# Kernel optimization log

Hardware: AMD Instinct MI355X
Metric: run time of the kernel (lower is better)

## Reference

```python
import jax, jax.numpy as jnp
import numpy as np
import math

FS = 44100.0
HOP = 256
N_BANDS = 24
KS_BUF = 768  # > max delay 44100/60 = 735 samples


def _lpc1(x, a):
    # order-1 all-pole (sample_wise_lpc with order 1, per-batch constant coeff):
    # y[n] = x[n] - a*y[n-1];  x: [B,N], a: [B]
    def step(yp, xt):
        y = xt - a * yp
        return y, y
    _, ys = jax.lax.scan(step, jnp.zeros_like(a), x.T)
    return ys.T


def _diff_ks(f0_frames, exc, l_b):
    # differentiable Karplus-Strong: fractional-delay loop + 2-tap damping filter.
    # f0_frames: [B,F] Hz, exc: [B,N], l_b: [B,F,2] (loop_coeff, loop_mix logits)
    B, N = exc.shape
    g = 0.999 * jax.nn.sigmoid(l_b[..., 0])   # loop gain in (0, 0.999)
    s = jax.nn.sigmoid(l_b[..., 1])           # loop-filter mix
    up = lambda p: jnp.repeat(p, HOP, axis=1)[:, :N]
    g_s, s_s = up(g), up(s)
    f0_s = up(jnp.clip(f0_frames, 60.0, None))
    D = jnp.clip(FS / f0_s, 2.0, 735.0)        # delay in samples
    Di = jnp.floor(D).astype(jnp.int32)
    fr = (D - Di).astype(exc.dtype)
    L = KS_BUF

    def step(carry, xs):
        buf, n = carry                         # buf: [B,L] circular delay line
        x_t, Di_t, fr_t, g_t, s_t = xs         # each [B]
        i1 = jnp.mod(n - Di_t, L)
        i2 = jnp.mod(n - Di_t - 1, L)
        i3 = jnp.mod(n - Di_t - 2, L)
        take = lambda i: jnp.take_along_axis(buf, i[:, None], axis=1)[:, 0]
        b1, b2, b3 = take(i1), take(i2), take(i3)
        z = (1.0 - fr_t) * b1 + fr_t * b2      # fractional-delay read y[n-D]
        z1 = (1.0 - fr_t) * b2 + fr_t * b3     # y[n-D-1]
        y = x_t + g_t * ((1.0 - s_t) * z + s_t * z1)
        buf = buf.at[:, jnp.mod(n, L)].set(y)
        return (buf, n + 1), y

    xs = (exc.T, Di.T, fr.T, g_s.T, s_s.T)
    init = (jnp.zeros((B, L), exc.dtype), jnp.int32(0))
    _, ys = jax.lax.scan(step, init, xs)
    return ys.T


def _body(x, body_gains):
    # bank of 24 two-pole resonators, log-spaced 80..8000 Hz, Q=10
    fc = jnp.geomspace(80.0, 8000.0, N_BANDS).astype(x.dtype)
    w = 2.0 * jnp.pi * fc / FS
    r = jnp.exp(-jnp.pi * fc / (10.0 * FS))
    a1 = -2.0 * r * jnp.cos(w)
    a2 = r * r
    b0 = 1.0 - r
    B = x.shape[0]

    def step(carry, xt):
        y1, y2 = carry                          # [B,24] each
        y = b0 * xt[:, None] - a1 * y1 - a2 * y2
        return (y, y1), jnp.sum(y * body_gains, axis=-1)

    init = (jnp.zeros((B, N_BANDS), x.dtype), jnp.zeros((B, N_BANDS), x.dtype))
    _, out = jax.lax.scan(step, init, x.T)
    return out.T


def _forward(excitation, pitch, w1, b1, w2, b2, excitation_gain, body_gains):
    B, _, N = excitation.shape
    h = jax.nn.relu(pitch @ w1.T + b1)
    mlp_out = h @ w2.T + b2                     # [B,3]
    loop_coeff = jnp.clip(mlp_out[:, 0], -2.0, 2.5)
    loop_mix = jnp.clip(mlp_out[:, 1], -2.5, 0.0)
    frames = N // HOP
    l_b = jnp.broadcast_to(jnp.stack([loop_coeff, loop_mix], -1)[:, None, :], (B, frames, 2))
    f0_frames = jnp.broadcast_to(pitch, (B, frames))
    exc_sq = (excitation * excitation_gain)[:, 0, :]
    f0_hz = jnp.clip(pitch[:, 0], 60.0, None)
    mult = jnp.clip(2.0 + 6.0 * (f0_hz - 60.0) / 600.0, 2.0, 8.0)
    cutoff = jnp.minimum(2.0 * jnp.pi * f0_hz * mult / FS, jnp.pi * 0.9)
    alpha = 1.0 - jnp.exp(-cutoff)
    exc_f = _lpc1(exc_sq * alpha[:, None], alpha - 1.0)   # pre-KS one-pole LP
    string = _diff_ks(f0_frames, exc_f, l_b)
    loop_post = jnp.clip(mlp_out[:, 2], -4.0, 4.0)
    cutoff_post = jnp.minimum(jnp.pi * jax.nn.sigmoid(loop_post), jnp.pi * 0.99)
    alpha_p = 1.0 - jnp.exp(-cutoff_post)
    string = _lpc1(string * alpha_p[:, None], alpha_p - 1.0)  # post one-pole LP
    out = _body(string, body_gains)
    return out[:, None, :], loop_coeff.mean(), loop_mix.mean(), loop_post.mean()


def setup_inputs():
    key = jax.random.key(0)
    k = jax.random.split(key, 6)
    B, N = 8, 32768
    excitation = jax.random.normal(k[0], (B, 1, N), dtype=jnp.float32)
    pitch = 60.0 + 600.0 * jax.random.uniform(k[1], (B, 1), dtype=jnp.float32)
    bnd1 = 0.1 * math.sqrt(6.0 / (1 + 16))   # xavier_uniform, gain 0.1
    bnd2 = 0.1 * math.sqrt(6.0 / (16 + 3))
    w1 = jax.random.uniform(k[2], (16, 1), jnp.float32, -bnd1, bnd1)
    b1 = jnp.zeros((16,), jnp.float32)
    w2 = jax.random.uniform(k[3], (3, 16), jnp.float32, -bnd2, bnd2)
    b2 = jnp.array([0.9, 0.0, 0.0], jnp.float32)
    excitation_gain = jnp.array(0.25, jnp.float32)
    body_gains = 0.006 * jnp.ones((1, N_BANDS), jnp.float32)
    return {"excitation": excitation, "pitch": pitch, "w1": w1, "b1": b1,
            "w2": w2, "b2": b2, "excitation_gain": excitation_gain,
            "body_gains": body_gains}


def reference(excitation, pitch, w1, b1, w2, b2, excitation_gain, body_gains):
    return _forward(excitation, pitch, w1, b1, w2, b2, excitation_gain, body_gains)
```

## Files before the change

### kernel.cpp

```cpp
#include <hip/hip_runtime.h>
#include <math.h>

#define NSAMP 32768
#define FS_F 44100.0f
#define PI_F 3.14159265358979323846f
#define T1 1024
#define FLAG_MAGIC 0x5A5A5A5A

struct BParams {
  float alpha, alpha_p;
  float fr, g, s;
  int Di;
  float lc, lm, lp;
};

__device__ inline float sigmoidf_(float x) { return 1.0f / (1.0f + expf(-x)); }

__device__ inline BParams compute_params(int b, const float* __restrict__ pitch,
                                         const float* __restrict__ w1,
                                         const float* __restrict__ b1,
                                         const float* __restrict__ w2,
                                         const float* __restrict__ b2) {
  BParams P;
  float p = pitch[b];
  float h[16];
#pragma unroll
  for (int i = 0; i < 16; ++i) {
    float v = fmaf(p, w1[i], b1[i]);
    h[i] = v > 0.0f ? v : 0.0f;
  }
  float m[3];
#pragma unroll
  for (int j = 0; j < 3; ++j) {
    float acc = b2[j];
#pragma unroll
    for (int i = 0; i < 16; ++i) acc = fmaf(h[i], w2[j * 16 + i], acc);
    m[j] = acc;
  }
  P.lc = fminf(fmaxf(m[0], -2.0f), 2.5f);
  P.lm = fminf(fmaxf(m[1], -2.5f), 0.0f);
  P.lp = fminf(fmaxf(m[2], -4.0f), 4.0f);
  P.g = 0.999f * sigmoidf_(P.lc);
  P.s = sigmoidf_(P.lm);
  float f0 = fmaxf(p, 60.0f);
  float D = fminf(fmaxf(FS_F / f0, 2.0f), 735.0f);
  int Di = (int)floorf(D);
  P.fr = D - (float)Di;
  P.Di = Di;
  float mult = fminf(fmaxf(2.0f + 6.0f * (f0 - 60.0f) / 600.0f, 2.0f), 8.0f);
  float cutoff = fminf(2.0f * PI_F * f0 * mult / FS_F, PI_F * 0.9f);
  P.alpha = 1.0f - expf(-cutoff);
  float cpost = fminf(PI_F * sigmoidf_(P.lp), PI_F * 0.99f);
  P.alpha_p = 1.0f - expf(-cpost);
  return P;
}

__device__ inline float rl63(float v) {
  return __int_as_float(__builtin_amdgcn_readlane(__float_as_int(v), 63));
}
__device__ inline float rlv(float v, int l) {
  return __int_as_float(__builtin_amdgcn_readlane(__float_as_int(v), l));
}
__device__ inline float shr1(float v, float bnd) {
  return __int_as_float(__builtin_amdgcn_update_dpp(
      __float_as_int(bnd), __float_as_int(v), 0x138 , 0xf, 0xf,
      false));
}
__device__ inline float ror1(float v) {
  return __int_as_float(__builtin_amdgcn_update_dpp(
      __float_as_int(v), __float_as_int(v), 0x13C , 0xf, 0xf,
      false));
}

__device__ inline void barrier_lgkm() {
  asm volatile("s_waitcnt lgkmcnt(0)\n\ts_barrier" ::: "memory");
}

__device__ inline void band_coef(int k, float& a1, float& a2, float& b0) {
  float fc = 80.0f * exp2f((float)k * (6.64385618977472436f / 23.0f));
  float w = 2.0f * PI_F * fc / FS_F;
  float r = expf(-PI_F * fc / (10.0f * FS_F));
  a1 = -2.0f * r * cosf(w);
  a2 = r * r;
  b0 = 1.0f - r;
}

__device__ inline void gen_tables(float* __restrict__ tabs, int W) {
  if (W >= 120) return;
  const int j = W / 5, sub = W % 5;
  float A1, A2, B0;
  band_coef(j, A1, A2, B0);
  if (sub == 0) *(float4*)&tabs[j * 4] = make_float4(A1, A2, B0, 0.f);
  float Q00 = -A1, Q01 = -A2, Q10 = 1.f, Q11 = 0.f;
#pragma unroll
  for (int sq = 0; sq < 2; ++sq) {
    float n00 = fmaf(Q00, Q00, Q01 * Q10);
    float n01 = fmaf(Q00, Q01, Q01 * Q11);
    float n10 = fmaf(Q10, Q00, Q11 * Q10);
    float n11 = fmaf(Q10, Q01, Q11 * Q11);
    Q00 = n00; Q01 = n01; Q10 = n10; Q11 = n11;
  }
  float K00 = Q00, K01 = Q01, K10 = Q10, K11 = Q11;
#pragma unroll
  for (int sq = 0; sq < 2; ++sq) {
    float n00 = fmaf(Q00, Q00, Q01 * Q10);
    float n01 = fmaf(Q00, Q01, Q01 * Q11);
    float n10 = fmaf(Q10, Q00, Q11 * Q10);
    float n11 = fmaf(Q10, Q01, Q11 * Q11);
    Q00 = n00; Q01 = n01; Q10 = n10; Q11 = n11;
  }
  float L00[7], L01[7], L10[7], L11[7];
  L00[0] = fmaf(Q00, K00, Q01 * K10);
  L01[0] = fmaf(Q00, K01, Q01 * K11);
  L10[0] = fmaf(Q10, K00, Q11 * K10);
  L11[0] = fmaf(Q10, K01, Q11 * K11);
#pragma unroll
  for (int k = 0; k < 6; ++k) {
    float s00 = fmaf(L00[k], L00[k], L01[k] * L10[k]);
    float s01 = fmaf(L00[k], L01[k], L01[k] * L11[k]);
    float s10 = fmaf(L10[k], L00[k], L11[k] * L10[k]);
    float s11 = fmaf(L10[k], L01[k], L11[k] * L11[k]);
    L00[k + 1] = s00; L01[k + 1] = s01; L10[k + 1] = s10; L11[k + 1] = s11;
  }
  if (sub == 0) {
#pragma unroll
    for (int k = 0; k < 6; ++k)
      *(float4*)&tabs[96 + (k * 24 + j) * 4] =
          make_float4(L00[k], L01[k], L10[k], L11[k]);
    *(float4*)&tabs[672 + j * 4] = make_float4(L00[6], L01[6], L10[6], L11[6]);
  }
  int l0 = sub * 13, l1 = l0 + 13;
  if (l1 > 64) l1 = 64;
  for (int l = l0; l < l1; ++l) {
    float R00 = 1.f, R01 = 0.f, R10 = 0.f, R11 = 1.f;
#pragma unroll
    for (int bit = 0; bit < 6; ++bit) {
      if ((l >> bit) & 1) {
        float n00 = fmaf(L00[bit], R00, L01[bit] * R10);
        float n01 = fmaf(L00[bit], R01, L01[bit] * R11);
        float n10 = fmaf(L10[bit], R00, L11[bit] * R10);
        float n11 = fmaf(L10[bit], R01, L11[bit] * R11);
        R00 = n00; R01 = n01; R10 = n10; R11 = n11;
      }
    }
    *(float4*)&tabs[768 + (j * 64 + l) * 4] = make_float4(R00, R01, R10, R11);
  }
}

struct SCtx {
  const float* exc_b;
  float scale, c;
  float m1, m2, m4, m8, m16, m32, c512, c2048, c8lane, cgk;
  float vrun;
  int s1;
  float* lws;
};

__device__ inline void ld2(const float* __restrict__ p, int g0, float4& a,
                           float4& b) {
  a = make_float4(0.f, 0.f, 0.f, 0.f);
  b = make_float4(0.f, 0.f, 0.f, 0.f);
  if (g0 >= 0 && g0 + 3 < NSAMP) a = *(const float4*)&p[g0];
  if (g0 + 4 >= 0 && g0 + 7 < NSAMP) b = *(const float4*)&p[g0 + 4];
}

__device__ inline void scan_seg_pre(SCtx& SC, float* xbuf, int seg, bool write,
                                    int t, float4 xa, float4 xb) {
  const int lane = t & 63, wid = t >> 6;
  const int rel0 = seg << 11;
  barrier_lgkm();
  const float c = SC.c, scale = SC.scale;
  float S = 0.0f;
  S = fmaf(c, S, scale * xa.x); S = fmaf(c, S, scale * xa.y);
  S = fmaf(c, S, scale * xa.z); S = fmaf(c, S, scale * xa.w);
  S = fmaf(c, S, scale * xb.x); S = fmaf(c, S, scale * xb.y);
  S = fmaf(c, S, scale * xb.z); S = fmaf(c, S, scale * xb.w);
  float Sw = S, u;
  u = __shfl_up(Sw, 1);  if (lane >= 1)  Sw = fmaf(SC.m1, u, Sw);
  u = __shfl_up(Sw, 2);  if (lane >= 2)  Sw = fmaf(SC.m2, u, Sw);
  u = __shfl_up(Sw, 4);  if (lane >= 4)  Sw = fmaf(SC.m4, u, Sw);
  u = __shfl_up(Sw, 8);  if (lane >= 8)  Sw = fmaf(SC.m8, u, Sw);
  u = __shfl_up(Sw, 16); if (lane >= 16) Sw = fmaf(SC.m16, u, Sw);
  u = __shfl_up(Sw, 32); if (lane >= 32) Sw = fmaf(SC.m32, u, Sw);
  if (lane == 63) SC.lws[wid] = Sw;
  barrier_lgkm();
  float a0 = SC.lws[0], a1w = SC.lws[1], a2w = SC.lws[2], a3w = SC.lws[3];
  float carry = (wid == 1)   ? a0
                : (wid == 2) ? fmaf(SC.c512, a0, a1w)
                : (wid == 3) ? fmaf(SC.c512, fmaf(SC.c512, a0, a1w), a2w)
                             : 0.0f;
  float Sprev = __shfl_up(Sw, 1);
  float Sex = (lane == 0) ? 0.0f : Sprev;
  Sex = fmaf(SC.c8lane, carry, Sex);
  float v = fmaf(SC.cgk, SC.vrun, Sex);
  float4 ya, yb;
  v = fmaf(c, v, scale * xa.x); ya.x = v;
  v = fmaf(c, v, scale * xa.y); ya.y = v;
  v = fmaf(c, v, scale * xa.z); ya.z = v;
  v = fmaf(c, v, scale * xa.w); ya.w = v;
  v = fmaf(c, v, scale * xb.x); yb.x = v;
  v = fmaf(c, v, scale * xb.y); yb.y = v;
  v = fmaf(c, v, scale * xb.z); yb.z = v;
  v = fmaf(c, v, scale * xb.w); yb.w = v;
  if (write) {
    int o = (rel0 + 8 * t) & 8191;
    *(float4*)&xbuf[o] = ya;
    *(float4*)&xbuf[o + 4] = yb;
    if (o < 768) {
      *(float4*)&xbuf[o + 8192] = ya;
      *(float4*)&xbuf[o + 4 + 8192] = yb;
    }
  }
  float tS = fmaf(SC.c512, fmaf(SC.c512, fmaf(SC.c512, a0, a1w), a2w), a3w);
  SC.vrun = fmaf(SC.c2048, SC.vrun, tS);
}

__device__ inline void w1_load(const float* __restrict__ xg, int s1, int seg,
                               int lane, float4* pf) {
  const int base = s1 + (seg << 11) + (lane << 5);
#pragma unroll
  for (int i = 0; i < 8; ++i) {
    const int g = base + 4 * i;
    float4 v = make_float4(0.f, 0.f, 0.f, 0.f);
    if (g >= 0 && g + 3 < NSAMP) v = *(const float4*)&xg[g];
    pf[i] = v;
  }
}

template <int KNUM>
__device__ void ks_wave0(float* __restrict__ yg, const float* xbuf, int lane,
                         int C, float c0w, float c1w, float c2w, int s1,
                         int n0, int end, int span, int nseg) {
  const int lq1 = (C - 1) - (KNUM - 1) * 64;
  const int W = n0 - s1;
  float yp[KNUM], xC[KNUM], xN[KNUM];
  float p1 = 0.f, p2 = 0.f;
  int rel = 0;
#pragma unroll
  for (int k = 0; k < KNUM; ++k) { yp[k] = 0.f; xC[k] = 0.f; xN[k] = 0.f; }
  for (int s = 0; s < nseg; ++s) {
    barrier_lgkm();
    if (s == 0) {
#pragma unroll
      for (int k = 0; k < KNUM; ++k) {
        int i = lane + (k << 6);
        xC[k] = xbuf[i];
        xN[k] = xbuf[C + i];
      }
    }
    int fence = (s + 1) << 11;
    if (fence > span) fence = span;
    while (rel + C <= W && rel < fence) {
      float b2v[KNUM], b3v[KNUM];
      b2v[0] = shr1(yp[0], p1);
#pragma unroll
      for (int k = 1; k < KNUM; ++k) b2v[k] = shr1(yp[k], ror1(yp[k - 1]));
      b3v[0] = shr1(b2v[0], p2);
#pragma unroll
      for (int k = 1; k < KNUM; ++k) b3v[k] = shr1(b2v[k], ror1(b2v[k - 1]));
      float p1n = rlv(yp[KNUM - 1], lq1);
      float p2n = rlv(b2v[KNUM - 1], lq1);
#pragma unroll
      for (int k = 0; k < KNUM; ++k)
        yp[k] = fmaf(c0w, yp[k], fmaf(c2w, b3v[k], fmaf(c1w, b2v[k], xC[k])));
      p1 = p1n;
      p2 = p2n;
      const float* xp = &xbuf[((rel + 2 * C) & 8191) + lane];
#pragma unroll
      for (int k = 0; k < KNUM; ++k) {
        xC[k] = xN[k];
        xN[k] = xp[k << 6];
      }
      rel += C;
    }
    while (rel < fence) {
      float b2v[KNUM], b3v[KNUM];
      b2v[0] = shr1(yp[0], p1);
#pragma unroll
      for (int k = 1; k < KNUM; ++k) b2v[k] = shr1(yp[k], ror1(yp[k - 1]));
      b3v[0] = shr1(b2v[0], p2);
#pragma unroll
      for (int k = 1; k < KNUM; ++k) b3v[k] = shr1(b2v[k], ror1(b2v[k - 1]));
      float p1n = rlv(yp[KNUM - 1], lq1);
      float p2n = rlv(b2v[KNUM - 1], lq1);
#pragma unroll
      for (int k = 0; k < KNUM; ++k)
        yp[k] = fmaf(c0w, yp[k], fmaf(c2w, b3v[k], fmaf(c1w, b2v[k], xC[k])));
      p1 = p1n;
      p2 = p2n;
#pragma unroll
      for (int k = 0; k < KNUM; ++k) {
        int i = lane + (k << 6);
        int n = s1 + rel + i;
        bool okl = (k < KNUM - 1) || (lane <= lq1);
        if (okl && n >= n0 && n < end) yg[n] = yp[k];
      }
      const float* xp = &xbuf[((rel + 2 * C) & 8191) + lane];
#pragma unroll
      for (int k = 0; k < KNUM; ++k) {
        xC[k] = xN[k];
        xN[k] = xp[k << 6];
      }
      rel += C;
    }
  }
}

__device__ inline void ks_phase(int b, int q, const BParams& P,
                                const float* __restrict__ exc, float scale0,
                                float* __restrict__ buf1, float* xbuf,
                                float* lws, float* tabs, int t) {
  const int C = P.Di;
  const int n0 = q << 10;
  float lg = -logf(P.g);
  int Wp = (int)ceilf(10.5f / fmaxf(lg, 1e-6f));
  if (Wp > 64) Wp = 64;
  if (Wp < 4) Wp = 4;
  int W = Wp * C;
  if (W > n0) W = n0;
  W = (W + 3) & ~3;
  const int s1 = n0 - W;
  const int span = W + T1;
  const int end = n0 + T1;
  const int nseg = (span + 2047) >> 11;
  float* yg = buf1 + (size_t)b * NSAMP;

  SCtx SC;
  SC.exc_b = exc + (size_t)b * NSAMP;
  SC.c = 1.0f - P.alpha;
  SC.scale = scale0 * P.alpha;
  {
    float c = SC.c;
    float c2v = c * c, c4 = c2v * c2v, c8 = c4 * c4;
    SC.m1 = c8;
    SC.m2 = SC.m1 * SC.m1;
    SC.m4 = SC.m2 * SC.m2;
    SC.m8 = SC.m4 * SC.m4;
    SC.m16 = SC.m8 * SC.m8;
    SC.m32 = SC.m16 * SC.m16;
    SC.c512 = SC.m32 * SC.m32;
    float c1024 = SC.c512 * SC.c512;
    SC.c2048 = c1024 * c1024;
    float l2c = log2f(c);
    SC.c8lane = exp2f((float)(8 * (t & 63)) * l2c);
    SC.cgk = exp2f((float)(8 * t) * l2c);
  }
  SC.vrun = 0.0f;
  SC.s1 = s1;
  SC.lws = lws;

  const float* xg = SC.exc_b;
  float4 pA0, pB0, pA1, pB1, pA2, pB2, pA3, pB3;
  ld2(xg, s1 - 2048 + 8 * t, pA0, pB0);
  ld2(xg, s1 + 8 * t, pA1, pB1);
  ld2(xg, s1 + 2048 + 8 * t, pA2, pB2);
  ld2(xg, s1 + 4096 + 8 * t, pA3, pB3);
  scan_seg_pre(SC, xbuf, -1, false, t, pA0, pB0);
  scan_seg_pre(SC, xbuf, 0, true, t, pA1, pB1);
  scan_seg_pre(SC, xbuf, 1, true, t, pA2, pB2);
  scan_seg_pre(SC, xbuf, 2, true, t, pA3, pB3);

  const float c0w = P.g * (1.0f - P.s) * (1.0f - P.fr);
  const float c1w = P.g * ((1.0f - P.s) * P.fr + P.s * (1.0f - P.fr));
  const float c2w = P.g * P.s * P.fr;
  const int lane = t & 63, wid = t >> 6;

  if (wid == 0) {
    switch ((C + 63) >> 6) {
      case 2:  ks_wave0<2>(yg, xbuf, lane, C, c0w, c1w, c2w, s1, n0, end, span, nseg); break;
      case 3:  ks_wave0<3>(yg, xbuf, lane, C, c0w, c1w, c2w, s1, n0, end, span, nseg); break;
      case 4:  ks_wave0<4>(yg, xbuf, lane, C, c0w, c1w, c2w, s1, n0, end, span, nseg); break;
      case 5:  ks_wave0<5>(yg, xbuf, lane, C, c0w, c1w, c2w, s1, n0, end, span, nseg); break;
      case 6:  ks_wave0<6>(yg, xbuf, lane, C, c0w, c1w, c2w, s1, n0, end, span, nseg); break;
      case 7:  ks_wave0<7>(yg, xbuf, lane, C, c0w, c1w, c2w, s1, n0, end, span, nseg); break;
      case 8:  ks_wave0<8>(yg, xbuf, lane, C, c0w, c1w, c2w, s1, n0, end, span, nseg); break;
      case 9:  ks_wave0<9>(yg, xbuf, lane, C, c0w, c1w, c2w, s1, n0, end, span, nseg); break;
      case 10: ks_wave0<10>(yg, xbuf, lane, C, c0w, c1w, c2w, s1, n0, end, span, nseg); break;
      case 11: ks_wave0<11>(yg, xbuf, lane, C, c0w, c1w, c2w, s1, n0, end, span, nseg); break;
      default: ks_wave0<12>(yg, xbuf, lane, C, c0w, c1w, c2w, s1, n0, end, span, nseg); break;
    }
  } else if (wid == 1) {
    const float c = SC.c, scale = SC.scale;
    const float n1 = SC.m4, n2 = SC.m8, n4 = SC.m16, n8 = SC.m32;
    const float n16 = SC.c512, n32 = SC.c512 * SC.c512;
    const float c2048 = SC.c2048;
    const float c32lane = exp2f((float)(lane << 5) * log2f(c));
    float vrun = SC.vrun;
    float4 pf[8];
    w1_load(xg, s1, 3, lane, pf);
    for (int s = 0; s < nseg; ++s) {
      barrier_lgkm();
      const int ls = s + 3;
      if (ls < nseg) {
        float S = 0.0f;
#pragma unroll
        for (int i = 0; i < 8; ++i) {
          S = fmaf(c, S, scale * pf[i].x);
          S = fmaf(c, S, scale * pf[i].y);
          S = fmaf(c, S, scale * pf[i].z);
          S = fmaf(c, S, scale * pf[i].w);
        }
        float Sw = S, u;
        u = __shfl_up(Sw, 1);  if (lane >= 1)  Sw = fmaf(n1, u, Sw);
        u = __shfl_up(Sw, 2);  if (lane >= 2)  Sw = fmaf(n2, u, Sw);
        u = __shfl_up(Sw, 4);  if (lane >= 4)  Sw = fmaf(n4, u, Sw);
        u = __shfl_up(Sw, 8);  if (lane >= 8)  Sw = fmaf(n8, u, Sw);
        u = __shfl_up(Sw, 16); if (lane >= 16) Sw = fmaf(n16, u, Sw);
        u = __shfl_up(Sw, 32); if (lane >= 32) Sw = fmaf(n32, u, Sw);
        float tot = rlv(Sw, 63);
        float Sex = __shfl_up(Sw, 1);
        if (lane == 0) Sex = 0.0f;
        float v = fmaf(c32lane, vrun, Sex);
        const int o = ((ls << 11) & 8191) + (lane << 5);
#pragma unroll
        for (int i = 0; i < 8; ++i) {
          float4 y;
          v = fmaf(c, v, scale * pf[i].x); y.x = v;
          v = fmaf(c, v, scale * pf[i].y); y.y = v;
          v = fmaf(c, v, scale * pf[i].z); y.z = v;
          v = fmaf(c, v, scale * pf[i].w); y.w = v;
          *(float4*)&xbuf[o + 4 * i] = y;
          if (o + 4 * i < 768) *(float4*)&xbuf[o + 4 * i + 8192] = y;
        }
        vrun = fmaf(c2048, vrun, tot);
        w1_load(xg, s1, ls + 1, lane, pf);
      }
    }
  } else {
    barrier_lgkm();
    gen_tables(tabs, (wid - 2) * 64 + lane);
    for (int s = 1; s < nseg; ++s) barrier_lgkm();
  }
}

__device__ inline void lpc_lds(const float* __restrict__ xg,
                               float* __restrict__ sl, int s2, int nt, int lim,
                               float scale, float c, int t, float* lws) {
  const int lane = t & 63, wid = t >> 6;
  float c2v = c * c, c4 = c2v * c2v, c8 = c4 * c4;
  float m1 = c8, m2 = m1 * m1, m4 = m2 * m2, m8 = m4 * m4, m16 = m8 * m8,
        m32 = m16 * m16;
  float c512 = m32 * m32;
  float c2048 = c512 * c512;
  c2048 *= c2048;
  float l2c = log2f(c);
  float c8lane = exp2f((float)(8 * lane) * l2c);
  float cgk = exp2f((float)(8 * t) * l2c);
  float vrun = 0.0f;
  for (int tile = 0; tile < nt; ++tile) {
    __syncthreads();
    int g0 = s2 + (tile << 11) + 8 * t;
    float4 xa = make_float4(0.f, 0.f, 0.f, 0.f);
    float4 xb = make_float4(0.f, 0.f, 0.f, 0.f);
    if (g0 + 3 < lim) xa = *(const float4*)&xg[g0];
    if (g0 + 7 < lim) xb = *(const float4*)&xg[g0 + 4];
    float S = 0.0f;
    S = fmaf(c, S, scale * xa.x); S = fmaf(c, S, scale * xa.y);
    S = fmaf(c, S, scale * xa.z); S = fmaf(c, S, scale * xa.w);
    S = fmaf(c, S, scale * xb.x); S = fmaf(c, S, scale * xb.y);
    S = fmaf(c, S, scale * xb.z); S = fmaf(c, S, scale * xb.w);
    float Sw = S, u;
    u = __shfl_up(Sw, 1);  if (lane >= 1)  Sw = fmaf(m1, u, Sw);
    u = __shfl_up(Sw, 2);  if (lane >= 2)  Sw = fmaf(m2, u, Sw);
    u = __shfl_up(Sw, 4);  if (lane >= 4)  Sw = fmaf(m4, u, Sw);
    u = __shfl_up(Sw, 8);  if (lane >= 8)  Sw = fmaf(m8, u, Sw);
    u = __shfl_up(Sw, 16); if (lane >= 16) Sw = fmaf(m16, u, Sw);
    u = __shfl_up(Sw, 32); if (lane >= 32) Sw = fmaf(m32, u, Sw);
    if (lane == 63) lws[wid] = Sw;
    __syncthreads();
    float a0 = lws[0], a1w = lws[1], a2w = lws[2], a3w = lws[3];
    float carry = (wid == 1)   ? a0
                  : (wid == 2) ? fmaf(c512, a0, a1w)
                  : (wid == 3) ? fmaf(c512, fmaf(c512, a0, a1w), a2w)
                               : 0.0f;
    float Sprev = __shfl_up(Sw, 1);
    float Sex = (lane == 0) ? 0.0f : Sprev;
    Sex = fmaf(c8lane, carry, Sex);
    float v = fmaf(cgk, vrun, Sex);
    int o = g0 - s2;
    float4 ya, yb;
    v = fmaf(c, v, scale * xa.x); ya.x = v;
    v = fmaf(c, v, scale * xa.y); ya.y = v;
    v = fmaf(c, v, scale * xa.z); ya.z = v;
    v = fmaf(c, v, scale * xa.w); ya.w = v;
    v = fmaf(c, v, scale * xb.x); yb.x = v;
    v = fmaf(c, v, scale * xb.y); yb.y = v;
    v = fmaf(c, v, scale * xb.z); yb.z = v;
    v = fmaf(c, v, scale * xb.w); yb.w = v;
    *(float4*)&sl[o] = ya;
    *(float4*)&sl[o + 4] = yb;
    float tS = fmaf(c512, fmaf(c512, fmaf(c512, a0, a1w), a2w), a3w);
    vrun = fmaf(c2048, vrun, tS);
  }
}

__device__ inline void body_phase(int b, int q, const BParams& P,
                                  const float* __restrict__ gains,
                                  const float* __restrict__ buf1,
                                  float* __restrict__ out, float* sl,
                                  float* lws, float (*lc0)[8],
                                  float (*lc1)[8], const float* tabs, int t) {
  const int lane = t & 63, wid = t >> 6;
  const int n0 = q << 10;
  const int base = n0 - 4096;
  int s2 = base - 256;
  if (s2 < 0) s2 = 0;
  const int end = n0 + 1024;
  const int nt = (end - s2 + 2047) >> 11;

  lpc_lds(buf1 + (size_t)b * NSAMP, sl, s2, nt, end, P.alpha_p,
          1.0f - P.alpha_p, t, lws);
  __syncthreads();

  const float* bandcL = tabs;
  const float* QlevL = tabs + 96;
  const float* QwL = tabs + 672;
  const float* RtabL = tabs + 768;

  const int tb = base + 20 * t;
  float4 acc[5];
#pragma unroll
  for (int i = 0; i < 5; ++i) acc[i] = make_float4(0.f, 0.f, 0.f, 0.f);

  for (int g = 0; g < 3; ++g) {
    float A1[8], A2[8], B0[8], GN[8];
#pragma unroll
    for (int j = 0; j < 8; ++j) {
      int k = g * 8 + j;
      float4 bc = *(const float4*)&bandcL[k * 4];
      A1[j] = bc.x; A2[j] = bc.y; B0[j] = bc.z;
      GN[j] = gains[k];
    }
    float cv0[8], cv1[8];
#pragma unroll
    for (int j = 0; j < 8; ++j) cv0[j] = cv1[j] = 0.f;
    for (int i = 0; i < 5; ++i) {
      int n = tb + 4 * i;
      float4 xv = make_float4(0.f, 0.f, 0.f, 0.f);
      if (n >= 0) xv = *(const float4*)&sl[n - s2];
#pragma unroll
      for (int e = 0; e < 4; ++e) {
        float xi = e == 0 ? xv.x : e == 1 ? xv.y : e == 2 ? xv.z : xv.w;
#pragma unroll
        for (int j = 0; j < 8; ++j) {
          float nc = fmaf(B0[j], xi, -fmaf(A1[j], cv0[j], A2[j] * cv1[j]));
          cv1[j] = cv0[j];
          cv0[j] = nc;
        }
      }
    }
    int kl = 0;
    for (int off = 1; off <= 32; off <<= 1, ++kl) {
      float q00[8], q01[8], q10[8], q11[8];
#pragma unroll
      for (int j = 0; j < 8; ++j) {
        float4 qv = *(const float4*)&QlevL[(kl * 24 + g * 8 + j) * 4];
        q00[j] = qv.x; q01[j] = qv.y; q10[j] = qv.z; q11[j] = qv.w;
      }
#pragma unroll
      for (int j = 0; j < 8; ++j) {
        float u0 = __shfl_up(cv0[j], off);
        float u1 = __shfl_up(cv1[j], off);
        if (lane >= off) {
          float nc0 = fmaf(q00[j], u0, fmaf(q01[j], u1, cv0[j]));
          float nc1 = fmaf(q10[j], u0, fmaf(q11[j], u1, cv1[j]));
          cv0[j] = nc0;
          cv1[j] = nc1;
        }
      }
    }
    __syncthreads();
    if (lane == 63) {
#pragma unroll
      for (int j = 0; j < 8; ++j) {
        lc0[wid][j] = cv0[j];
        lc1[wid][j] = cv1[j];
      }
    }
    __syncthreads();
    float qw00[8], qw01[8], qw10[8], qw11[8];
#pragma unroll
    for (int j = 0; j < 8; ++j) {
      float4 qv = *(const float4*)&QwL[(g * 8 + j) * 4];
      qw00[j] = qv.x; qw01[j] = qv.y; qw10[j] = qv.z; qw11[j] = qv.w;
    }
    float car0[8], car1[8];
#pragma unroll
    for (int j = 0; j < 8; ++j) car0[j] = car1[j] = 0.f;
    for (int v = 0; v < wid; ++v) {
#pragma unroll
      for (int j = 0; j < 8; ++j) {
        float n0c = fmaf(qw00[j], car0[j], fmaf(qw01[j], car1[j], lc0[v][j]));
        float n1c = fmaf(qw10[j], car0[j], fmaf(qw11[j], car1[j], lc1[v][j]));
        car0[j] = n0c;
        car1[j] = n1c;
      }
    }
    float y1[8], y2[8];
#pragma unroll
    for (int j = 0; j < 8; ++j) {
      float4 rv = *(const float4*)&RtabL[((g * 8 + j) * 64 + lane) * 4];
      float e0 = __shfl_up(cv0[j], 1);
      float e1 = __shfl_up(cv1[j], 1);
      if (lane == 0) { e0 = 0.f; e1 = 0.f; }
      y1[j] = fmaf(rv.x, car0[j], fmaf(rv.y, car1[j], e0));
      y2[j] = fmaf(rv.z, car0[j], fmaf(rv.w, car1[j], e1));
    }
    if (tb + 20 > n0) {
      for (int i = 0; i < 5; ++i) {
        float4 xv = *(const float4*)&sl[tb - s2 + 4 * i];
        float4 ov = acc[i];
#pragma unroll
        for (int e = 0; e < 4; ++e) {
          float xi = e == 0 ? xv.x : e == 1 ? xv.y : e == 2 ? xv.z : xv.w;
          float a = 0.f;
#pragma unroll
          for (int j = 0; j < 8; ++j) {
            float yv = fmaf(B0[j], xi, -fmaf(A1[j], y1[j], A2[j] * y2[j]));
            y2[j] = y1[j];
            y1[j] = yv;
            a = fmaf(GN[j], yv, a);
          }
          if (e == 0) ov.x += a;
          else if (e == 1) ov.y += a;
          else if (e == 2) ov.z += a;
          else ov.w += a;
        }
        acc[i] = ov;
      }
    }
  }
  if (tb + 20 > n0) {
    float* outb = out + (size_t)b * NSAMP;
#pragma unroll
    for (int i = 0; i < 5; ++i) {
      int n = tb + 4 * i;
      if (n >= n0) *(float4*)&outb[n] = acc[i];
    }
  }
}

__global__ void __launch_bounds__(256, 1) synth_all(
    const float* __restrict__ exc, const float* __restrict__ pitch,
    const float* __restrict__ w1, const float* __restrict__ b1,
    const float* __restrict__ w2, const float* __restrict__ b2,
    const float* __restrict__ eg, const float* __restrict__ gains,
    float* __restrict__ buf1, int* __restrict__ flags,
    float* __restrict__ out) {
  const int blk = blockIdx.x;
  const int b = blk >> 5, q = blk & 31;
  const int t = threadIdx.x;
  __shared__ __align__(16) float smem[15888];

  BParams P = compute_params(b, pitch, w1, b1, w2, b2);
  if (blk == 0 && t < 64) {
    int bb = (t < 8) ? t : 0;
    BParams Q = compute_params(bb, pitch, w1, b1, w2, b2);
    float slc = 0.f, slm = 0.f, slp = 0.f;
    for (int i = 0; i < 8; ++i) {
      slc += rlv(Q.lc, i);
      slm += rlv(Q.lm, i);
      slp += rlv(Q.lp, i);
    }
    if (t == 0) {
      out[8 * NSAMP + 0] = slc / 8.0f;
      out[8 * NSAMP + 1] = slm / 8.0f;
      out[8 * NSAMP + 2] = slp / 8.0f;
    }
  }

  ks_phase(b, q, P, exc, eg[0], buf1, smem, smem + 8960, smem + 8976, t);
  __syncthreads();

  const int n0 = q << 10;
  int s2 = n0 - 4096 - 256;
  if (s2 < 0) s2 = 0;
  const int qlo = s2 >> 10;
  if (t == 0) {
    __hip_atomic_store(&flags[blk], FLAG_MAGIC, __ATOMIC_RELEASE,
                       __HIP_MEMORY_SCOPE_AGENT);
    for (int f = qlo; f < q; ++f) {
      while (__hip_atomic_load(&flags[b * 32 + f], __ATOMIC_ACQUIRE,
                               __HIP_MEMORY_SCOPE_AGENT) != FLAG_MAGIC) {
        __builtin_amdgcn_s_sleep(8);
      }
    }
  }
  __syncthreads();

  body_phase(b, q, P, gains, buf1, out, smem, smem + 6144,
             (float(*)[8])(smem + 6152), (float(*)[8])(smem + 6184),
             smem + 8976, t);
}

extern "C" void kernel_launch(void* const* d_in, const int* in_sizes, int n_in,
                              void* d_out, int out_size, void* d_ws, size_t ws_size,
                              hipStream_t stream) {
  const float* exc = (const float*)d_in[0];
  const float* pitch = (const float*)d_in[1];
  const float* w1 = (const float*)d_in[2];
  const float* b1 = (const float*)d_in[3];
  const float* w2 = (const float*)d_in[4];
  const float* b2 = (const float*)d_in[5];
  const float* eg = (const float*)d_in[6];
  const float* bg = (const float*)d_in[7];
  float* out = (float*)d_out;
  float* buf1 = (float*)d_ws;
  int* flags = (int*)(buf1 + 8 * NSAMP);

  hipLaunchKernelGGL(synth_all, dim3(256), dim3(256), 0, stream, exc, pitch,
                     w1, b1, w2, b2, eg, bg, buf1, flags, out);
}
```

Baseline: 114.4 us.

## Precompute full LPC-filtered excitation into large LDS before Karplus-Strong loop

Replaces the per-segment producer/consumer pipeline, in which wave 1 scanned the LPC filter into an 8K ring buffer while wave 0 ran the KS recurrence with per-segment barriers, with a two-pass parallel scan. All four waves first compute the whole filtered excitation span into a ~131KB dynamic LDS buffer, then apply inter-segment carry corrections. Only after that does wave 0 run the KS loop, with no barriers and no ring-buffer wrap. This removes barrier stalls and ring indexing from the serial loop. In exchange the LPC work is no longer overlapped with the KS recurrence, and the kernel now needs much more LDS.

```diff
diff --git a/kernel.cpp b/kernel.cpp
--- a/kernel.cpp
+++ b/kernel.cpp
@@ -6,6 +6,11 @@
 #define PI_F 3.14159265358979323846f
 #define T1 1024
 #define FLAG_MAGIC 0x5A5A5A5A
+
+#define XCAP 33536
+#define LWS_OFF 33536
+#define TABS_OFF 33568
+#define SMEM_FLOATS 40480
 
 struct BParams {
   float alpha, alpha_p;
@@ -55,9 +60,6 @@
   return P;
 }
 
-__device__ inline float rl63(float v) {
-  return __int_as_float(__builtin_amdgcn_readlane(__float_as_int(v), 63));
-}
 __device__ inline float rlv(float v, int l) {
   return __int_as_float(__builtin_amdgcn_readlane(__float_as_int(v), l));
 }
@@ -70,10 +72,6 @@
   return __int_as_float(__builtin_amdgcn_update_dpp(
       __float_as_int(v), __float_as_int(v), 0x13C , 0xf, 0xf,
       false));
-}
-
-__device__ inline void barrier_lgkm() {
-  asm volatile("s_waitcnt lgkmcnt(0)\n\ts_barrier" ::: "memory");
 }
 
 __device__ inline void band_coef(int k, float& a1, float& a2, float& b0) {
@@ -147,168 +145,91 @@
   }
 }
 
-struct SCtx {
-  const float* exc_b;
-  float scale, c;
-  float m1, m2, m4, m8, m16, m32, c512, c2048, c8lane, cgk;
-  float vrun;
-  int s1;
-  float* lws;
-};
-
-__device__ inline void ld2(const float* __restrict__ p, int g0, float4& a,
-                           float4& b) {
-  a = make_float4(0.f, 0.f, 0.f, 0.f);
-  b = make_float4(0.f, 0.f, 0.f, 0.f);
-  if (g0 >= 0 && g0 + 3 < NSAMP) a = *(const float4*)&p[g0];
-  if (g0 + 4 >= 0 && g0 + 7 < NSAMP) b = *(const float4*)&p[g0 + 4];
-}
-
-__device__ inline void scan_seg_pre(SCtx& SC, float* xbuf, int seg, bool write,
-                                    int t, float4 xa, float4 xb) {
-  const int lane = t & 63, wid = t >> 6;
-  const int rel0 = seg << 11;
-  barrier_lgkm();
-  const float c = SC.c, scale = SC.scale;
-  float S = 0.0f;
-  S = fmaf(c, S, scale * xa.x); S = fmaf(c, S, scale * xa.y);
-  S = fmaf(c, S, scale * xa.z); S = fmaf(c, S, scale * xa.w);
-  S = fmaf(c, S, scale * xb.x); S = fmaf(c, S, scale * xb.y);
-  S = fmaf(c, S, scale * xb.z); S = fmaf(c, S, scale * xb.w);
-  float Sw = S, u;
-  u = __shfl_up(Sw, 1);  if (lane >= 1)  Sw = fmaf(SC.m1, u, Sw);
-  u = __shfl_up(Sw, 2);  if (lane >= 2)  Sw = fmaf(SC.m2, u, Sw);
-  u = __shfl_up(Sw, 4);  if (lane >= 4)  Sw = fmaf(SC.m4, u, Sw);
-  u = __shfl_up(Sw, 8);  if (lane >= 8)  Sw = fmaf(SC.m8, u, Sw);
-  u = __shfl_up(Sw, 16); if (lane >= 16) Sw = fmaf(SC.m16, u, Sw);
-  u = __shfl_up(Sw, 32); if (lane >= 32) Sw = fmaf(SC.m32, u, Sw);
-  if (lane == 63) SC.lws[wid] = Sw;
-  barrier_lgkm();
-  float a0 = SC.lws[0], a1w = SC.lws[1], a2w = SC.lws[2], a3w = SC.lws[3];
-  float carry = (wid == 1)   ? a0
-                : (wid == 2) ? fmaf(SC.c512, a0, a1w)
-                : (wid == 3) ? fmaf(SC.c512, fmaf(SC.c512, a0, a1w), a2w)
-                             : 0.0f;
-  float Sprev = __shfl_up(Sw, 1);
-  float Sex = (lane == 0) ? 0.0f : Sprev;
-  Sex = fmaf(SC.c8lane, carry, Sex);
-  float v = fmaf(SC.cgk, SC.vrun, Sex);
-  float4 ya, yb;
-  v = fmaf(c, v, scale * xa.x); ya.x = v;
-  v = fmaf(c, v, scale * xa.y); ya.y = v;
-  v = fmaf(c, v, scale * xa.z); ya.z = v;
-  v = fmaf(c, v, scale * xa.w); ya.w = v;
-  v = fmaf(c, v, scale * xb.x); yb.x = v;
-  v = fmaf(c, v, scale * xb.y); yb.y = v;
-  v = fmaf(c, v, scale * xb.z); yb.z = v;
-  v = fmaf(c, v, scale * xb.w); yb.w = v;
-  if (write) {
-    int o = (rel0 + 8 * t) & 8191;
-    *(float4*)&xbuf[o] = ya;
-    *(float4*)&xbuf[o + 4] = yb;
-    if (o < 768) {
-      *(float4*)&xbuf[o + 8192] = ya;
-      *(float4*)&xbuf[o + 4 + 8192] = yb;
-    }
-  }
-  float tS = fmaf(SC.c512, fmaf(SC.c512, fmaf(SC.c512, a0, a1w), a2w), a3w);
-  SC.vrun = fmaf(SC.c2048, SC.vrun, tS);
-}
-
-__device__ inline void w1_load(const float* __restrict__ xg, int s1, int seg,
-                               int lane, float4* pf) {
-  const int base = s1 + (seg << 11) + (lane << 5);
-#pragma unroll
-  for (int i = 0; i < 8; ++i) {
-    const int g = base + 4 * i;
-    float4 v = make_float4(0.f, 0.f, 0.f, 0.f);
-    if (g >= 0 && g + 3 < NSAMP) v = *(const float4*)&xg[g];
-    pf[i] = v;
-  }
-}
-
 template <int KNUM>
-__device__ void ks_wave0(float* __restrict__ yg, const float* xbuf, int lane,
+__device__ void ks_wave0(float* __restrict__ yg, const float* xall, int lane,
                          int C, float c0w, float c1w, float c2w, int s1,
-                         int n0, int end, int span, int nseg) {
+                         int n0, int end, int span) {
   const int lq1 = (C - 1) - (KNUM - 1) * 64;
   const int W = n0 - s1;
   float yp[KNUM], xC[KNUM], xN[KNUM];
   float p1 = 0.f, p2 = 0.f;
+#pragma unroll
+  for (int k = 0; k < KNUM; ++k) {
+    yp[k] = 0.f;
+    xC[k] = xall[lane + (k << 6)];
+    xN[k] = xall[C + lane + (k << 6)];
+  }
   int rel = 0;
-#pragma unroll
-  for (int k = 0; k < KNUM; ++k) { yp[k] = 0.f; xC[k] = 0.f; xN[k] = 0.f; }
-  for (int s = 0; s < nseg; ++s) {
-    barrier_lgkm();
-    if (s == 0) {
-#pragma unroll
-      for (int k = 0; k < KNUM; ++k) {
-        int i = lane + (k << 6);
-        xC[k] = xbuf[i];
-        xN[k] = xbuf[C + i];
-      }
-    }
-    int fence = (s + 1) << 11;
-    if (fence > span) fence = span;
-    while (rel + C <= W && rel < fence) {
-      float b2v[KNUM], b3v[KNUM];
-      b2v[0] = shr1(yp[0], p1);
-#pragma unroll
-      for (int k = 1; k < KNUM; ++k) b2v[k] = shr1(yp[k], ror1(yp[k - 1]));
-      b3v[0] = shr1(b2v[0], p2);
-#pragma unroll
-      for (int k = 1; k < KNUM; ++k) b3v[k] = shr1(b2v[k], ror1(b2v[k - 1]));
-      float p1n = rlv(yp[KNUM - 1], lq1);
-      float p2n = rlv(b2v[KNUM - 1], lq1);
-#pragma unroll
-      for (int k = 0; k < KNUM; ++k)
-        yp[k] = fmaf(c0w, yp[k], fmaf(c2w, b3v[k], fmaf(c1w, b2v[k], xC[k])));
-      p1 = p1n;
-      p2 = p2n;
-      const float* xp = &xbuf[((rel + 2 * C) & 8191) + lane];
+  while (rel + C <= W) {
+    float b2v[KNUM], b3v[KNUM];
+    b2v[0] = shr1(yp[0], p1);
+#pragma unroll
+    for (int k = 1; k < KNUM; ++k) b2v[k] = shr1(yp[k], ror1(yp[k - 1]));
+    b3v[0] = shr1(b2v[0], p2);
+#pragma unroll
+    for (int k = 1; k < KNUM; ++k) b3v[k] = shr1(b2v[k], ror1(b2v[k - 1]));
+    float p1n = rlv(yp[KNUM - 1], lq1);
+    float p2n = rlv(b2v[KNUM - 1], lq1);
+#pragma unroll
+    for (int k = 0; k < KNUM; ++k)
+      yp[k] = fmaf(c0w, yp[k], fmaf(c2w, b3v[k], fmaf(c1w, b2v[k], xC[k])));
+    p1 = p1n;
+    p2 = p2n;
+    int r2 = rel + 2 * C;
+    if (r2 < span) {
+      const float* xp = &xall[r2 + lane];
 #pragma unroll
       for (int k = 0; k < KNUM; ++k) {
         xC[k] = xN[k];
         xN[k] = xp[k << 6];
       }
-      rel += C;
-    }
-    while (rel < fence) {
-      float b2v[KNUM], b3v[KNUM];
-      b2v[0] = shr1(yp[0], p1);
-#pragma unroll
-      for (int k = 1; k < KNUM; ++k) b2v[k] = shr1(yp[k], ror1(yp[k - 1]));
-      b3v[0] = shr1(b2v[0], p2);
-#pragma unroll
-      for (int k = 1; k < KNUM; ++k) b3v[k] = shr1(b2v[k], ror1(b2v[k - 1]));
-      float p1n = rlv(yp[KNUM - 1], lq1);
-      float p2n = rlv(b2v[KNUM - 1], lq1);
-#pragma unroll
-      for (int k = 0; k < KNUM; ++k)
-        yp[k] = fmaf(c0w, yp[k], fmaf(c2w, b3v[k], fmaf(c1w, b2v[k], xC[k])));
-      p1 = p1n;
-      p2 = p2n;
-#pragma unroll
-      for (int k = 0; k < KNUM; ++k) {
-        int i = lane + (k << 6);
-        int n = s1 + rel + i;
-        bool okl = (k < KNUM - 1) || (lane <= lq1);
-        if (okl && n >= n0 && n < end) yg[n] = yp[k];
-      }
-      const float* xp = &xbuf[((rel + 2 * C) & 8191) + lane];
+    } else {
+#pragma unroll
+      for (int k = 0; k < KNUM; ++k) xC[k] = xN[k];
+    }
+    rel += C;
+  }
+  while (rel < span) {
+    float b2v[KNUM], b3v[KNUM];
+    b2v[0] = shr1(yp[0], p1);
+#pragma unroll
+    for (int k = 1; k < KNUM; ++k) b2v[k] = shr1(yp[k], ror1(yp[k - 1]));
+    b3v[0] = shr1(b2v[0], p2);
+#pragma unroll
+    for (int k = 1; k < KNUM; ++k) b3v[k] = shr1(b2v[k], ror1(b2v[k - 1]));
+    float p1n = rlv(yp[KNUM - 1], lq1);
+    float p2n = rlv(b2v[KNUM - 1], lq1);
+#pragma unroll
+    for (int k = 0; k < KNUM; ++k)
+      yp[k] = fmaf(c0w, yp[k], fmaf(c2w, b3v[k], fmaf(c1w, b2v[k], xC[k])));
+    p1 = p1n;
+    p2 = p2n;
+#pragma unroll
+    for (int k = 0; k < KNUM; ++k) {
+      int i = lane + (k << 6);
+      int n = s1 + rel + i;
+      bool okl = (k < KNUM - 1) || (lane <= lq1);
+      if (okl && n >= n0 && n < end) yg[n] = yp[k];
+    }
+    int r2 = rel + 2 * C;
+    if (r2 < span) {
+      const float* xp = &xall[r2 + lane];
 #pragma unroll
       for (int k = 0; k < KNUM; ++k) {
         xC[k] = xN[k];
         xN[k] = xp[k << 6];
       }
-      rel += C;
-    }
+    } else {
+#pragma unroll
+      for (int k = 0; k < KNUM; ++k) xC[k] = xN[k];
+    }
+    rel += C;
   }
 }
 
 __device__ inline void ks_phase(int b, int q, const BParams& P,
                                 const float* __restrict__ exc, float scale0,
-                                float* __restrict__ buf1, float* xbuf,
+                                float* __restrict__ buf1, float* xall,
                                 float* lws, float* tabs, int t) {
   const int C = P.Di;
   const int n0 = q << 10;
@@ -322,114 +243,122 @@
   const int s1 = n0 - W;
   const int span = W + T1;
   const int end = n0 + T1;
-  const int nseg = (span + 2047) >> 11;
+  const int NSG = (span + 2047) >> 11;
   float* yg = buf1 + (size_t)b * NSAMP;
-
-  SCtx SC;
-  SC.exc_b = exc + (size_t)b * NSAMP;
-  SC.c = 1.0f - P.alpha;
-  SC.scale = scale0 * P.alpha;
+  const float* xg = exc + (size_t)b * NSAMP;
+
+  const float c = 1.0f - P.alpha;
+  const float scale = scale0 * P.alpha;
+  const float c2v = c * c, c4 = c2v * c2v, c8 = c4 * c4, c16 = c8 * c8;
+  const float c32 = c16 * c16, c64 = c32 * c32, c128 = c64 * c64;
+  const float c256 = c128 * c128, c512 = c256 * c256, c1024 = c512 * c512;
+  const float c2048 = c1024 * c1024;
+  const int lane = t & 63, wid = t >> 6;
+  const float c32lane = exp2f((float)(lane << 5) * log2f(c));
+
+  for (int r = 0; r < 5; ++r) {
+    int si = r * 4 + wid;
+    if (si > NSG) break;
+    int sg = si - 1;
+    int gbase = s1 + (sg << 11) + (lane << 5);
+    float4 pf[8];
+#pragma unroll
+    for (int i = 0; i < 8; ++i) {
+      int g = gbase + 4 * i;
+      float4 v = make_float4(0.f, 0.f, 0.f, 0.f);
+      if (g >= 0 && g + 3 < NSAMP) v = *(const float4*)&xg[g];
+      pf[i] = v;
+    }
+    float S = 0.0f;
+#pragma unroll
+    for (int i = 0; i < 8; ++i) {
+      S = fmaf(c, S, scale * pf[i].x);
+      S = fmaf(c, S, scale * pf[i].y);
+      S = fmaf(c, S, scale * pf[i].z);
+      S = fmaf(c, S, scale * pf[i].w);
+    }
+    float Sw = S, u;
+    u = __shfl_up(Sw, 1);  if (lane >= 1)  Sw = fmaf(c32, u, Sw);
+    u = __shfl_up(Sw, 2);  if (lane >= 2)  Sw = fmaf(c64, u, Sw);
+    u = __shfl_up(Sw, 4);  if (lane >= 4)  Sw = fmaf(c128, u, Sw);
+    u = __shfl_up(Sw, 8);  if (lane >= 8)  Sw = fmaf(c256, u, Sw);
+    u = __shfl_up(Sw, 16); if (lane >= 16) Sw = fmaf(c512, u, Sw);
+    u = __shfl_up(Sw, 32); if (lane >= 32) Sw = fmaf(c1024, u, Sw);
+    float tot = rlv(Sw, 63);
+    float Sex = __shfl_up(Sw, 1);
+    if (lane == 0) Sex = 0.0f;
+    if (lane == 0) lws[si] = tot;
+    if (sg >= 0) {
+      float v = Sex;
+#pragma unroll
+      for (int i = 0; i < 8; ++i) {
+        float4 y;
+        v = fmaf(c, v, scale * pf[i].x); y.x = v;
+        v = fmaf(c, v, scale * pf[i].y); y.y = v;
+        v = fmaf(c, v, scale * pf[i].z); y.z = v;
+        v = fmaf(c, v, scale * pf[i].w); y.w = v;
+        pf[i] = y;
+      }
+      int o = (sg << 11) + (lane << 5);
+#pragma unroll
+      for (int i = 0; i < 8; ++i) {
+        int ci = (lane + i) & 7;
+        *(float4*)&xall[o + 4 * ci] = pf[ci];
+      }
+    }
+  }
+  if (4 * t < 768) {
+    *(float4*)&xall[(NSG << 11) + 4 * t] = make_float4(0.f, 0.f, 0.f, 0.f);
+  }
+  __syncthreads();
   {
-    float c = SC.c;
-    float c2v = c * c, c4 = c2v * c2v, c8 = c4 * c4;
-    SC.m1 = c8;
-    SC.m2 = SC.m1 * SC.m1;
-    SC.m4 = SC.m2 * SC.m2;
-    SC.m8 = SC.m4 * SC.m4;
-    SC.m16 = SC.m8 * SC.m8;
-    SC.m32 = SC.m16 * SC.m16;
-    SC.c512 = SC.m32 * SC.m32;
-    float c1024 = SC.c512 * SC.c512;
-    SC.c2048 = c1024 * c1024;
-    float l2c = log2f(c);
-    SC.c8lane = exp2f((float)(8 * (t & 63)) * l2c);
-    SC.cgk = exp2f((float)(8 * t) * l2c);
-  }
-  SC.vrun = 0.0f;
-  SC.s1 = s1;
-  SC.lws = lws;
-
-  const float* xg = SC.exc_b;
-  float4 pA0, pB0, pA1, pB1, pA2, pB2, pA3, pB3;
-  ld2(xg, s1 - 2048 + 8 * t, pA0, pB0);
-  ld2(xg, s1 + 8 * t, pA1, pB1);
-  ld2(xg, s1 + 2048 + 8 * t, pA2, pB2);
-  ld2(xg, s1 + 4096 + 8 * t, pA3, pB3);
-  scan_seg_pre(SC, xbuf, -1, false, t, pA0, pB0);
-  scan_seg_pre(SC, xbuf, 0, true, t, pA1, pB1);
-  scan_seg_pre(SC, xbuf, 1, true, t, pA2, pB2);
-  scan_seg_pre(SC, xbuf, 2, true, t, pA3, pB3);
+    float p4[8];
+    p4[0] = 1.0f;
+#pragma unroll
+    for (int i = 1; i < 8; ++i) p4[i] = p4[i - 1] * c4;
+    for (int r = 0; r < 5; ++r) {
+      int si = r * 4 + wid;
+      if (si > NSG) break;
+      int sg = si - 1;
+      if (sg < 0) continue;
+      float vr = 0.0f;
+      for (int i = 0; i < si; ++i) vr = fmaf(c2048, vr, lws[i]);
+      float corr0 = c * (c32lane * vr);
+      int o = (sg << 11) + (lane << 5);
+#pragma unroll
+      for (int i = 0; i < 8; ++i) {
+        int ci = (lane + i) & 7;
+        float4 y = *(float4*)&xall[o + 4 * ci];
+        float f = corr0 * p4[ci];
+        y.x += f; f *= c;
+        y.y += f; f *= c;
+        y.z += f; f *= c;
+        y.w += f;
+        *(float4*)&xall[o + 4 * ci] = y;
+      }
+    }
+  }
+  __syncthreads();
 
   const float c0w = P.g * (1.0f - P.s) * (1.0f - P.fr);
   const float c1w = P.g * ((1.0f - P.s) * P.fr + P.s * (1.0f - P.fr));
   const float c2w = P.g * P.s * P.fr;
-  const int lane = t & 63, wid = t >> 6;
-
   if (wid == 0) {
     switch ((C + 63) >> 6) {
-      case 2:  ks_wave0<2>(yg, xbuf, lane, C, c0w, c1w, c2w, s1, n0, end, span, nseg); break;
-      case 3:  ks_wave0<3>(yg, xbuf, lane, C, c0w, c1w, c2w, s1, n0, end, span, nseg); break;
-      case 4:  ks_wave0<4>(yg, xbuf, lane, C, c0w, c1w, c2w, s1, n0, end, span, nseg); break;
-      case 5:  ks_wave0<5>(yg, xbuf, lane, C, c0w, c1w, c2w, s1, n0, end, span, nseg); break;
-      case 6:  ks_wave0<6>(yg, xbuf, lane, C, c0w, c1w, c2w, s1, n0, end, span, nseg); break;
-      case 7:  ks_wave0<7>(yg, xbuf, lane, C, c0w, c1w, c2w, s1, n0, end, span, nseg); break;
-      case 8:  ks_wave0<8>(yg, xbuf, lane, C, c0w, c1w, c2w, s1, n0, end, span, nseg); break;
-      case 9:  ks_wave0<9>(yg, xbuf, lane, C, c0w, c1w, c2w, s1, n0, end, span, nseg); break;
-      case 10: ks_wave0<10>(yg, xbuf, lane, C, c0w, c1w, c2w, s1, n0, end, span, nseg); break;
-      case 11: ks_wave0<11>(yg, xbuf, lane, C, c0w, c1w, c2w, s1, n0, end, span, nseg); break;
-      default: ks_wave0<12>(yg, xbuf, lane, C, c0w, c1w, c2w, s1, n0, end, span, nseg); break;
-    }
-  } else if (wid == 1) {
-    const float c = SC.c, scale = SC.scale;
-    const float n1 = SC.m4, n2 = SC.m8, n4 = SC.m16, n8 = SC.m32;
-    const float n16 = SC.c512, n32 = SC.c512 * SC.c512;
-    const float c2048 = SC.c2048;
-    const float c32lane = exp2f((float)(lane << 5) * log2f(c));
-    float vrun = SC.vrun;
-    float4 pf[8];
-    w1_load(xg, s1, 3, lane, pf);
-    for (int s = 0; s < nseg; ++s) {
-      barrier_lgkm();
-      const int ls = s + 3;
-      if (ls < nseg) {
-        float S = 0.0f;
-#pragma unroll
-        for (int i = 0; i < 8; ++i) {
-          S = fmaf(c, S, scale * pf[i].x);
-          S = fmaf(c, S, scale * pf[i].y);
-          S = fmaf(c, S, scale * pf[i].z);
-          S = fmaf(c, S, scale * pf[i].w);
-        }
-        float Sw = S, u;
-        u = __shfl_up(Sw, 1);  if (lane >= 1)  Sw = fmaf(n1, u, Sw);
-        u = __shfl_up(Sw, 2);  if (lane >= 2)  Sw = fmaf(n2, u, Sw);
-        u = __shfl_up(Sw, 4);  if (lane >= 4)  Sw = fmaf(n4, u, Sw);
-        u = __shfl_up(Sw, 8);  if (lane >= 8)  Sw = fmaf(n8, u, Sw);
-        u = __shfl_up(Sw, 16); if (lane >= 16) Sw = fmaf(n16, u, Sw);
-        u = __shfl_up(Sw, 32); if (lane >= 32) Sw = fmaf(n32, u, Sw);
-        float tot = rlv(Sw, 63);
-        float Sex = __shfl_up(Sw, 1);
-        if (lane == 0) Sex = 0.0f;
-        float v = fmaf(c32lane, vrun, Sex);
-        const int o = ((ls << 11) & 8191) + (lane << 5);
-#pragma unroll
-        for (int i = 0; i < 8; ++i) {
-          float4 y;
-          v = fmaf(c, v, scale * pf[i].x); y.x = v;
-          v = fmaf(c, v, scale * pf[i].y); y.y = v;
-          v = fmaf(c, v, scale * pf[i].z); y.z = v;
-          v = fmaf(c, v, scale * pf[i].w); y.w = v;
-          *(float4*)&xbuf[o + 4 * i] = y;
-          if (o + 4 * i < 768) *(float4*)&xbuf[o + 4 * i + 8192] = y;
-        }
-        vrun = fmaf(c2048, vrun, tot);
-        w1_load(xg, s1, ls + 1, lane, pf);
-      }
-    }
-  } else {
-    barrier_lgkm();
+      case 2:  ks_wave0<2>(yg, xall, lane, C, c0w, c1w, c2w, s1, n0, end, span); break;
+      case 3:  ks_wave0<3>(yg, xall, lane, C, c0w, c1w, c2w, s1, n0, end, span); break;
+      case 4:  ks_wave0<4>(yg, xall, lane, C, c0w, c1w, c2w, s1, n0, end, span); break;
+      case 5:  ks_wave0<5>(yg, xall, lane, C, c0w, c1w, c2w, s1, n0, end, span); break;
+      case 6:  ks_wave0<6>(yg, xall, lane, C, c0w, c1w, c2w, s1, n0, end, span); break;
+      case 7:  ks_wave0<7>(yg, xall, lane, C, c0w, c1w, c2w, s1, n0, end, span); break;
+      case 8:  ks_wave0<8>(yg, xall, lane, C, c0w, c1w, c2w, s1, n0, end, span); break;
+      case 9:  ks_wave0<9>(yg, xall, lane, C, c0w, c1w, c2w, s1, n0, end, span); break;
+      case 10: ks_wave0<10>(yg, xall, lane, C, c0w, c1w, c2w, s1, n0, end, span); break;
+      case 11: ks_wave0<11>(yg, xall, lane, C, c0w, c1w, c2w, s1, n0, end, span); break;
+      default: ks_wave0<12>(yg, xall, lane, C, c0w, c1w, c2w, s1, n0, end, span); break;
+    }
+  } else if (wid >= 2) {
     gen_tables(tabs, (wid - 2) * 64 + lane);
-    for (int s = 1; s < nseg; ++s) barrier_lgkm();
   }
 }
 
@@ -647,10 +576,10 @@
     const float* __restrict__ eg, const float* __restrict__ gains,
     float* __restrict__ buf1, int* __restrict__ flags,
     float* __restrict__ out) {
+  extern __shared__ float smem[];
   const int blk = blockIdx.x;
   const int b = blk >> 5, q = blk & 31;
   const int t = threadIdx.x;
-  __shared__ __align__(16) float smem[15888];
 
   BParams P = compute_params(b, pitch, w1, b1, w2, b2);
   if (blk == 0 && t < 64) {
@@ -669,7 +598,7 @@
     }
   }
 
-  ks_phase(b, q, P, exc, eg[0], buf1, smem, smem + 8960, smem + 8976, t);
+  ks_phase(b, q, P, exc, eg[0], buf1, smem, smem + LWS_OFF, smem + TABS_OFF, t);
   __syncthreads();
 
   const int n0 = q << 10;
@@ -690,7 +619,7 @@
 
   body_phase(b, q, P, gains, buf1, out, smem, smem + 6144,
              (float(*)[8])(smem + 6152), (float(*)[8])(smem + 6184),
-             smem + 8976, t);
+             smem + TABS_OFF, t);
 }
 
 extern "C" void kernel_launch(void* const* d_in, const int* in_sizes, int n_in,
@@ -708,6 +637,13 @@
   float* buf1 = (float*)d_ws;
   int* flags = (int*)(buf1 + 8 * NSAMP);
 
-  hipLaunchKernelGGL(synth_all, dim3(256), dim3(256), 0, stream, exc, pitch,
-                     w1, b1, w2, b2, eg, bg, buf1, flags, out);
-}
+  static int lds_set = 0;
+  if (!lds_set) {
+    hipFuncSetAttribute(reinterpret_cast<const void*>(synth_all),
+                        hipFuncAttributeMaxDynamicSharedMemorySize,
+                        SMEM_FLOATS * 4);
+    lds_set = 1;
+  }
+  hipLaunchKernelGGL(synth_all, dim3(256), dim3(256), SMEM_FLOATS * 4, stream,
+                     exc, pitch, w1, b1, w2, b2, eg, bg, buf1, flags, out);
+}
```

Result: slower. 126.7 us (+10.8%).
